# Optimization experiments

Hardware: AMD Instinct MI355X
Metric: run time of the kernel (lower is better)

Reference implementation:

```python
import jax, jax.numpy as jnp
import numpy as np

NUM_EXPERTS = 8
TOP_K = 2
HIDDEN = 2048
INTER = 2816  # 2*INTER = 5632 fused gate+up
NUM_TOKENS = 8192


def setup_inputs() -> dict:
    key = jax.random.key(0)
    k1, k2, k3, k4 = jax.random.split(key, 4)
    hidden_states = jax.random.normal(k1, (NUM_TOKENS, HIDDEN), dtype=jnp.float32)
    gate_w = jax.random.normal(k2, (NUM_EXPERTS, HIDDEN), dtype=jnp.float32) * 0.02
    w13 = jax.random.normal(k3, (NUM_EXPERTS, 2 * INTER, HIDDEN), dtype=jnp.float32) * 0.02
    w2 = jax.random.normal(k4, (NUM_EXPERTS, HIDDEN, INTER), dtype=jnp.float32) * 0.02
    return {"hidden_states": hidden_states, "gate_w": gate_w, "w13": w13, "w2": w2}


def reference(hidden_states, gate_w, w13, w2):
    x = hidden_states  # [T, H]
    # Gate: ReplicatedLinear (no bias) -> router logits [T, E]
    router_logits = jnp.einsum('th,eh->te', x, gate_w)
    probs = jax.nn.softmax(router_logits, axis=-1)
    # top-k routing, renormalize=False: use softmax probs directly
    topk_vals, topk_idx = jax.lax.top_k(probs, TOP_K)  # [T, K]
    # combine weights [T, E]: sum of one-hot(topk_idx) * topk_vals
    cw = jnp.sum(jax.nn.one_hot(topk_idx, NUM_EXPERTS, dtype=x.dtype) * topk_vals[..., None], axis=1)
    # Dense per-expert grouped GEMM, masked combine (E is small and fixed)
    out = jnp.zeros_like(x)
    for e in range(NUM_EXPERTS):
        gu = jnp.einsum('th,ih->ti', x, w13[e])          # [T, 2I]
        g, u = gu[:, :INTER], gu[:, INTER:]
        h = jax.nn.silu(g) * u                            # SiLU-gated
        y = jnp.einsum('ti,hi->th', h, w2[e])             # [T, H]
        out = out + cw[:, e:e + 1] * y
    return out
```

## Files before the change

### kernel.cpp

```cpp
#include <hip/hip_runtime.h>
#include <stdint.h>
#include <stddef.h>

#define NE 8
#define HIDDEN 2048
#define INTER 2816
#define NT 8192
#define NROWS (NT * 2)

typedef __bf16 bf16x8 __attribute__((ext_vector_type(8)));
typedef float f32x4 __attribute__((ext_vector_type(4)));

__device__ __forceinline__ unsigned short f2bf(float f) {
  union { float f; uint32_t u; } v; v.f = f;
  uint32_t r = v.u + 0x7FFFu + ((v.u >> 16) & 1u);
  return (unsigned short)(r >> 16);
}

__device__ __forceinline__ void async16(const void* g, const unsigned short* lds_ptr) {
  __builtin_amdgcn_global_load_lds(
      (const __attribute__((address_space(1))) uint32_t*)g,
      (__attribute__((address_space(3))) uint32_t*)lds_ptr,
      16, 0, 0);
}

__global__ void cvt_kernel(const float4* __restrict__ src, ushort4* __restrict__ dst) {
  size_t i = (size_t)blockIdx.x * blockDim.x + threadIdx.x;
  float4 v = src[i];
  ushort4 o;
  o.x = f2bf(v.x); o.y = f2bf(v.y); o.z = f2bf(v.z); o.w = f2bf(v.w);
  dst[i] = o;
}

__global__ __launch_bounds__(256) void router_kernel(
    const float* __restrict__ x, const float* __restrict__ gw,
    int* __restrict__ top_e, float* __restrict__ top_w, int* __restrict__ counts) {
  int t = blockIdx.x * 4 + (threadIdx.x >> 6);
  int lane = threadIdx.x & 63;
  const float* xr = x + (size_t)t * HIDDEN;
  float acc[NE];
#pragma unroll
  for (int e = 0; e < NE; ++e) acc[e] = 0.f;
  for (int kb = 0; kb < HIDDEN; kb += 64) {
    float xv = xr[kb + lane];
#pragma unroll
    for (int e = 0; e < NE; ++e) acc[e] += xv * gw[e * HIDDEN + kb + lane];
  }
#pragma unroll
  for (int e = 0; e < NE; ++e) {
#pragma unroll
    for (int off = 32; off > 0; off >>= 1) acc[e] += __shfl_xor(acc[e], off, 64);
  }
  if (lane == 0) {
    float mx = acc[0];
#pragma unroll
    for (int e = 1; e < NE; ++e) mx = fmaxf(mx, acc[e]);
    float p[NE];
    float s = 0.f;
#pragma unroll
    for (int e = 0; e < NE; ++e) { p[e] = expf(acc[e] - mx); s += p[e]; }
    int e1 = 0;
#pragma unroll
    for (int e = 1; e < NE; ++e) if (p[e] > p[e1]) e1 = e;
    int e2 = (e1 == 0) ? 1 : 0;
#pragma unroll
    for (int e = 0; e < NE; ++e) if (e != e1 && p[e] > p[e2]) e2 = e;
    float inv = 1.f / s;
    top_e[2 * t] = e1; top_e[2 * t + 1] = e2;
    top_w[2 * t] = p[e1] * inv; top_w[2 * t + 1] = p[e2] * inv;
    atomicAdd(&counts[e1], 1);
    atomicAdd(&counts[e2], 1);
  }
}

__global__ void scan_kernel(const int* __restrict__ counts, int* __restrict__ offs) {
  if (threadIdx.x == 0) {
    int s = 0;
    for (int e = 0; e < NE; ++e) { offs[e] = s; s += counts[e]; }
    offs[NE] = s;
  }
}

__global__ void fill_kernel(const int* __restrict__ top_e, const float* __restrict__ top_w,
                            const int* __restrict__ offs, int* __restrict__ fillc,
                            int* __restrict__ row_tok, float* __restrict__ row_w,
                            int* __restrict__ row_of) {
  int t = blockIdx.x * 256 + threadIdx.x;
#pragma unroll
  for (int j = 0; j < 2; ++j) {
    int e = top_e[2 * t + j];
    int slot = atomicAdd(&fillc[e], 1);
    int row = offs[e] + slot;
    row_tok[row] = t;
    row_w[row] = top_w[2 * t + j];
    row_of[2 * t + j] = row;
  }
}

__global__ __launch_bounds__(512, 2) void gemm1_kernel(
    const unsigned short* __restrict__ xb, const unsigned short* __restrict__ w13b,
    const int* __restrict__ row_tok, const int* __restrict__ offs,
    unsigned short* __restrict__ hbuf) {
  __shared__ __align__(16) unsigned short smem[2][2][16384];
  const int e = blockIdx.z, mt = blockIdx.y, nt = blockIdx.x;
  const int row0 = offs[e];
  const int cnt = offs[e + 1] - row0;
  if (mt * 256 >= cnt) return;
  const int tid = threadIdx.x;

  const int lrow = tid >> 2;
  const int gch = ((tid & 3) ^ ((lrow >> 1) & 3)) * 8;
  size_t aA[2];
#pragma unroll
  for (int i = 0; i < 2; ++i) {
    int grow = mt * 256 + i * 128 + lrow;
    int rr = row0 + (grow < cnt ? grow : cnt - 1);
    aA[i] = (size_t)row_tok[rr] * HIDDEN + gch;
  }
  const size_t aBg = ((size_t)e * 2 * INTER + nt * 128 + lrow) * (size_t)HIDDEN + gch;
  const size_t aBu = ((size_t)e * 2 * INTER + INTER + nt * 128 + lrow) * (size_t)HIDDEN + gch;

  const int wv = tid >> 6, wm = wv >> 1, wn = wv & 1;
  const int l = tid & 63, lm = l & 15, lq = l >> 4;
  const int loff = lm * 32 + ((lq ^ ((lm >> 1) & 3)) * 8);

  f32x4 accg[4][4], accu[4][4];
#pragma unroll
  for (int i = 0; i < 4; ++i)
#pragma unroll
    for (int j = 0; j < 4; ++j) {
      accg[i][j] = (f32x4){0.f, 0.f, 0.f, 0.f};
      accu[i][j] = (f32x4){0.f, 0.f, 0.f, 0.f};
    }

#define ST_A1(NB, KH, KT) do { \
    size_t ko = (size_t)(KT) * 64 + (KH) * 32; \
    async16(xb + aA[0] + ko, &smem[NB][KH][tid * 8]); \
    async16(xb + aA[1] + ko, &smem[NB][KH][4096 + tid * 8]); } while (0)
#define ST_B1(NB, KH, KT) do { \
    size_t ko = (size_t)(KT) * 64 + (KH) * 32; \
    async16(w13b + aBg + ko, &smem[NB][KH][8192 + tid * 8]); \
    async16(w13b + aBu + ko, &smem[NB][KH][12288 + tid * 8]); } while (0)

  ST_A1(0, 0, 0); ST_B1(0, 0, 0); ST_A1(0, 1, 0); ST_B1(0, 1, 0);
  asm volatile("s_waitcnt vmcnt(4)" ::: "memory");
  __builtin_amdgcn_s_barrier();

  const int NTK = HIDDEN / 64;
  for (int t = 0; t < NTK; ++t) {
    const int b = t & 1, nb = b ^ 1;
    const bool pf = (t + 1 < NTK);
#pragma unroll
    for (int kk = 0; kk < 2; ++kk) {
      const unsigned short* sK = &smem[b][kk][0];
      bf16x8 af[4], bfr[4];
#pragma unroll
      for (int i = 0; i < 4; ++i)
        af[i] = *(const bf16x8*)(sK + (wm * 64 + i * 16) * 32 + loff);
#pragma unroll
      for (int j = 0; j < 4; ++j)
        bfr[j] = *(const bf16x8*)(sK + (256 + wn * 64 + j * 16) * 32 + loff);
      if (pf) ST_A1(nb, kk, t + 1);
      __builtin_amdgcn_s_barrier();
      asm volatile("s_waitcnt lgkmcnt(0)" ::: "memory");
      __builtin_amdgcn_sched_barrier(0);
      __builtin_amdgcn_s_setprio(1);
#pragma unroll
      for (int i = 0; i < 4; ++i)
#pragma unroll
        for (int j = 0; j < 4; ++j)
          accg[i][j] = __builtin_amdgcn_mfma_f32_16x16x32_bf16(af[i], bfr[j], accg[i][j], 0, 0, 0);
      __builtin_amdgcn_s_setprio(0);
      __builtin_amdgcn_s_barrier();
#pragma unroll
      for (int j = 0; j < 4; ++j)
        bfr[j] = *(const bf16x8*)(sK + (384 + wn * 64 + j * 16) * 32 + loff);
      if (pf) ST_B1(nb, kk, t + 1);
      if (kk == 0) {
        if (pf) { asm volatile("s_waitcnt vmcnt(4)" ::: "memory"); }
        else    { asm volatile("s_waitcnt vmcnt(0)" ::: "memory"); }
      } else if (pf) {
        asm volatile("s_waitcnt vmcnt(4)" ::: "memory");
      }
      __builtin_amdgcn_s_barrier();
      asm volatile("s_waitcnt lgkmcnt(0)" ::: "memory");
      __builtin_amdgcn_sched_barrier(0);
      __builtin_amdgcn_s_setprio(1);
#pragma unroll
      for (int i = 0; i < 4; ++i)
#pragma unroll
        for (int j = 0; j < 4; ++j)
          accu[i][j] = __builtin_amdgcn_mfma_f32_16x16x32_bf16(af[i], bfr[j], accu[i][j], 0, 0, 0);
      __builtin_amdgcn_s_setprio(0);
      __builtin_amdgcn_s_barrier();
    }
  }
#undef ST_A1
#undef ST_B1

#pragma unroll
  for (int i = 0; i < 4; ++i) {
#pragma unroll
    for (int r = 0; r < 4; ++r) {
      int grow = mt * 256 + wm * 64 + i * 16 + lq * 4 + r;
      if (grow < cnt) {
        size_t hrow = (size_t)(row0 + grow) * INTER + nt * 128 + wn * 64 + lm;
#pragma unroll
        for (int j = 0; j < 4; ++j) {
          float g = accg[i][j][r], u = accu[i][j][r];
          float sg = g / (1.f + expf(-g));
          hbuf[hrow + j * 16] = f2bf(sg * u);
        }
      }
    }
  }
}

__global__ __launch_bounds__(512, 2) void gemm2_kernel(
    const unsigned short* __restrict__ hbuf, const unsigned short* __restrict__ w2b,
    const float* __restrict__ row_w, const int* __restrict__ offs,
    float* __restrict__ ybuf) {
  __shared__ __align__(16) unsigned short smem[2][2][16384];
  const int e = blockIdx.z, mt = blockIdx.y, nt = blockIdx.x;
  const int row0 = offs[e];
  const int cnt = offs[e + 1] - row0;
  if (mt * 256 >= cnt) return;
  const int tid = threadIdx.x;

  const int lrow = tid >> 2;
  const int gch = ((tid & 3) ^ ((lrow >> 1) & 3)) * 8;
  size_t aA[2], aB[2];
#pragma unroll
  for (int i = 0; i < 2; ++i) {
    int grow = mt * 256 + i * 128 + lrow;
    int rr = row0 + (grow < cnt ? grow : cnt - 1);
    aA[i] = (size_t)rr * INTER + gch;
    aB[i] = ((size_t)e * HIDDEN + nt * 256 + i * 128 + lrow) * (size_t)INTER + gch;
  }

  const int wv = tid >> 6, wm = wv >> 1, wn = wv & 1;
  const int l = tid & 63, lm = l & 15, lq = l >> 4;
  const int loff = lm * 32 + ((lq ^ ((lm >> 1) & 3)) * 8);

  f32x4 acc[4][8];
#pragma unroll
  for (int i = 0; i < 4; ++i)
#pragma unroll
    for (int j = 0; j < 8; ++j) acc[i][j] = (f32x4){0.f, 0.f, 0.f, 0.f};

#define ST_A2(NB, KH, KT) do { \
    size_t ko = (size_t)(KT) * 64 + (KH) * 32; \
    async16(hbuf + aA[0] + ko, &smem[NB][KH][tid * 8]); \
    async16(hbuf + aA[1] + ko, &smem[NB][KH][4096 + tid * 8]); } while (0)
#define ST_B2(NB, KH, KT) do { \
    size_t ko = (size_t)(KT) * 64 + (KH) * 32; \
    async16(w2b + aB[0] + ko, &smem[NB][KH][8192 + tid * 8]); \
    async16(w2b + aB[1] + ko, &smem[NB][KH][12288 + tid * 8]); } while (0)

  ST_A2(0, 0, 0); ST_B2(0, 0, 0); ST_A2(0, 1, 0); ST_B2(0, 1, 0);
  asm volatile("s_waitcnt vmcnt(4)" ::: "memory");
  __builtin_amdgcn_s_barrier();

  const int NTK = INTER / 64;
  for (int t = 0; t < NTK; ++t) {
    const int b = t & 1, nb = b ^ 1;
    const bool pf = (t + 1 < NTK);
#pragma unroll
    for (int kk = 0; kk < 2; ++kk) {
      const unsigned short* sK = &smem[b][kk][0];
      bf16x8 af[4], bfr[4];
#pragma unroll
      for (int i = 0; i < 4; ++i)
        af[i] = *(const bf16x8*)(sK + (wm * 64 + i * 16) * 32 + loff);
#pragma unroll
      for (int j = 0; j < 4; ++j)
        bfr[j] = *(const bf16x8*)(sK + (256 + wn * 128 + j * 16) * 32 + loff);
      if (pf) ST_A2(nb, kk, t + 1);
      __builtin_amdgcn_s_barrier();
      asm volatile("s_waitcnt lgkmcnt(0)" ::: "memory");
      __builtin_amdgcn_sched_barrier(0);
      __builtin_amdgcn_s_setprio(1);
#pragma unroll
      for (int i = 0; i < 4; ++i)
#pragma unroll
        for (int j = 0; j < 4; ++j)
          acc[i][j] = __builtin_amdgcn_mfma_f32_16x16x32_bf16(af[i], bfr[j], acc[i][j], 0, 0, 0);
      __builtin_amdgcn_s_setprio(0);
      __builtin_amdgcn_s_barrier();
#pragma unroll
      for (int j = 0; j < 4; ++j)
        bfr[j] = *(const bf16x8*)(sK + (256 + wn * 128 + (j + 4) * 16) * 32 + loff);
      if (pf) ST_B2(nb, kk, t + 1);
      if (kk == 0) {
        if (pf) { asm volatile("s_waitcnt vmcnt(4)" ::: "memory"); }
        else    { asm volatile("s_waitcnt vmcnt(0)" ::: "memory"); }
      } else if (pf) {
        asm volatile("s_waitcnt vmcnt(4)" ::: "memory");
      }
      __builtin_amdgcn_s_barrier();
      asm volatile("s_waitcnt lgkmcnt(0)" ::: "memory");
      __builtin_amdgcn_sched_barrier(0);
      __builtin_amdgcn_s_setprio(1);
#pragma unroll
      for (int i = 0; i < 4; ++i)
#pragma unroll
        for (int j = 0; j < 4; ++j)
          acc[i][j + 4] = __builtin_amdgcn_mfma_f32_16x16x32_bf16(af[i], bfr[j], acc[i][j + 4], 0, 0, 0);
      __builtin_amdgcn_s_setprio(0);
      __builtin_amdgcn_s_barrier();
    }
  }
#undef ST_A2
#undef ST_B2

#pragma unroll
  for (int i = 0; i < 4; ++i) {
#pragma unroll
    for (int r = 0; r < 4; ++r) {
      int grow = mt * 256 + wm * 64 + i * 16 + lq * 4 + r;
      if (grow < cnt) {
        int rr = row0 + grow;
        float w = row_w[rr];
        float* yrow = ybuf + (size_t)rr * HIDDEN + nt * 256 + wn * 128 + lm;
#pragma unroll
        for (int j = 0; j < 8; ++j) yrow[j * 16] = w * acc[i][j][r];
      }
    }
  }
}

__global__ __launch_bounds__(256) void combine_kernel(
    const float* __restrict__ ybuf, const int* __restrict__ row_of,
    float* __restrict__ out) {
  int t = blockIdx.x;
  int r0 = row_of[2 * t], r1 = row_of[2 * t + 1];
  const float4* y0 = (const float4*)(ybuf + (size_t)r0 * HIDDEN);
  const float4* y1 = (const float4*)(ybuf + (size_t)r1 * HIDDEN);
  float4* o = (float4*)(out + (size_t)t * HIDDEN);
#pragma unroll
  for (int it = 0; it < 2; ++it) {
    int c = it * 256 + threadIdx.x;
    float4 a = y0[c], b = y1[c];
    o[c] = make_float4(a.x + b.x, a.y + b.y, a.z + b.z, a.w + b.w);
  }
}

extern "C" void kernel_launch(void* const* d_in, const int* in_sizes, int n_in,
                              void* d_out, int out_size, void* d_ws, size_t ws_size,
                              hipStream_t stream) {
  const float* x = (const float*)d_in[0];
  const float* gw = (const float*)d_in[1];
  const float* w13 = (const float*)d_in[2];
  const float* w2 = (const float*)d_in[3];
  float* out = (float*)d_out;
  char* ws = (char*)d_ws;

  int* counts = (int*)(ws + 0);
  int* fillc = (int*)(ws + 32);
  int* offs = (int*)(ws + 64);
  int* top_e = (int*)(ws + 1024);
  float* top_w = (float*)(ws + 66560);
  int* row_tok = (int*)(ws + 132096);
  float* row_w = (float*)(ws + 197632);
  int* row_of = (int*)(ws + 263168);
  unsigned short* xb = (unsigned short*)(ws + 328704);
  unsigned short* w13b = (unsigned short*)(ws + 33883136);
  float* ybuf = (float*)(ws + 33883136);
  unsigned short* w2b = (unsigned short*)(ws + 218432512);
  unsigned short* hb = (unsigned short*)(ws + 310707200);

  hipMemsetAsync(ws, 0, 1024, stream);

  cvt_kernel<<<16384, 256, 0, stream>>>((const float4*)x, (ushort4*)xb);
  cvt_kernel<<<90112, 256, 0, stream>>>((const float4*)w13, (ushort4*)w13b);
  cvt_kernel<<<45056, 256, 0, stream>>>((const float4*)w2, (ushort4*)w2b);

  router_kernel<<<2048, 256, 0, stream>>>(x, gw, top_e, top_w, counts);
  scan_kernel<<<1, 64, 0, stream>>>(counts, offs);
  fill_kernel<<<32, 256, 0, stream>>>(top_e, top_w, offs, fillc, row_tok, row_w, row_of);

  gemm1_kernel<<<dim3(22, 32, 8), 512, 0, stream>>>(xb, w13b, row_tok, offs, hb);
  gemm2_kernel<<<dim3(8, 32, 8), 512, 0, stream>>>(hb, w2b, row_w, offs, ybuf);
  combine_kernel<<<8192, 256, 0, stream>>>(ybuf, row_of, out);
}
```

Before: 1.644 ms.

## Switch both GEMM mainloops to a 4-stage ring buffer with prefetch three slices ahead

```diff
diff --git a/kernel.cpp b/kernel.cpp
--- a/kernel.cpp
+++ b/kernel.cpp
@@ -101,7 +101,7 @@
     const unsigned short* __restrict__ xb, const unsigned short* __restrict__ w13b,
     const int* __restrict__ row_tok, const int* __restrict__ offs,
     unsigned short* __restrict__ hbuf) {
-  __shared__ __align__(16) unsigned short smem[2][2][16384];
+  __shared__ __align__(16) unsigned short smem[4][16384];
   const int e = blockIdx.z, mt = blockIdx.y, nt = blockIdx.x;
   const int row0 = offs[e];
   const int cnt = offs[e + 1] - row0;
@@ -133,67 +133,60 @@
       accu[i][j] = (f32x4){0.f, 0.f, 0.f, 0.f};
     }
 
-#define ST_A1(NB, KH, KT) do { \
-    size_t ko = (size_t)(KT) * 64 + (KH) * 32; \
-    async16(xb + aA[0] + ko, &smem[NB][KH][tid * 8]); \
-    async16(xb + aA[1] + ko, &smem[NB][KH][4096 + tid * 8]); } while (0)
-#define ST_B1(NB, KH, KT) do { \
-    size_t ko = (size_t)(KT) * 64 + (KH) * 32; \
-    async16(w13b + aBg + ko, &smem[NB][KH][8192 + tid * 8]); \
-    async16(w13b + aBu + ko, &smem[NB][KH][12288 + tid * 8]); } while (0)
-
-  ST_A1(0, 0, 0); ST_B1(0, 0, 0); ST_A1(0, 1, 0); ST_B1(0, 1, 0);
-  asm volatile("s_waitcnt vmcnt(4)" ::: "memory");
+#define ST_A1(P) do { \
+    size_t ko = (size_t)(P) * 32; unsigned short* sD = &smem[(P) & 3][0]; \
+    async16(xb + aA[0] + ko, sD + tid * 8); \
+    async16(xb + aA[1] + ko, sD + 4096 + tid * 8); } while (0)
+#define ST_B1(P) do { \
+    size_t ko = (size_t)(P) * 32; unsigned short* sD = &smem[(P) & 3][0]; \
+    async16(w13b + aBg + ko, sD + 8192 + tid * 8); \
+    async16(w13b + aBu + ko, sD + 12288 + tid * 8); } while (0)
+
+  const int NP = HIDDEN / 32;
+  ST_A1(0); ST_B1(0); ST_A1(1); ST_B1(1); ST_A1(2); ST_B1(2);
+  asm volatile("s_waitcnt vmcnt(8)" ::: "memory");
   __builtin_amdgcn_s_barrier();
 
-  const int NTK = HIDDEN / 64;
-  for (int t = 0; t < NTK; ++t) {
-    const int b = t & 1, nb = b ^ 1;
-    const bool pf = (t + 1 < NTK);
-#pragma unroll
-    for (int kk = 0; kk < 2; ++kk) {
-      const unsigned short* sK = &smem[b][kk][0];
-      bf16x8 af[4], bfr[4];
-#pragma unroll
-      for (int i = 0; i < 4; ++i)
-        af[i] = *(const bf16x8*)(sK + (wm * 64 + i * 16) * 32 + loff);
+  for (int p = 0; p < NP; ++p) {
+    const unsigned short* sK = &smem[p & 3][0];
+    const bool pf = (p + 3 < NP);
+    bf16x8 af[4], bfr[4];
+#pragma unroll
+    for (int i = 0; i < 4; ++i)
+      af[i] = *(const bf16x8*)(sK + (wm * 64 + i * 16) * 32 + loff);
+#pragma unroll
+    for (int j = 0; j < 4; ++j)
+      bfr[j] = *(const bf16x8*)(sK + (256 + wn * 64 + j * 16) * 32 + loff);
+    if (pf) ST_A1(p + 3);
+    __builtin_amdgcn_s_barrier();
+    asm volatile("s_waitcnt lgkmcnt(0)" ::: "memory");
+    __builtin_amdgcn_sched_barrier(0);
+    __builtin_amdgcn_s_setprio(1);
+#pragma unroll
+    for (int i = 0; i < 4; ++i)
 #pragma unroll
       for (int j = 0; j < 4; ++j)
-        bfr[j] = *(const bf16x8*)(sK + (256 + wn * 64 + j * 16) * 32 + loff);
-      if (pf) ST_A1(nb, kk, t + 1);
-      __builtin_amdgcn_s_barrier();
-      asm volatile("s_waitcnt lgkmcnt(0)" ::: "memory");
-      __builtin_amdgcn_sched_barrier(0);
-      __builtin_amdgcn_s_setprio(1);
-#pragma unroll
-      for (int i = 0; i < 4; ++i)
-#pragma unroll
-        for (int j = 0; j < 4; ++j)
-          accg[i][j] = __builtin_amdgcn_mfma_f32_16x16x32_bf16(af[i], bfr[j], accg[i][j], 0, 0, 0);
-      __builtin_amdgcn_s_setprio(0);
-      __builtin_amdgcn_s_barrier();
+        accg[i][j] = __builtin_amdgcn_mfma_f32_16x16x32_bf16(af[i], bfr[j], accg[i][j], 0, 0, 0);
+    __builtin_amdgcn_s_setprio(0);
+    __builtin_amdgcn_s_barrier();
+#pragma unroll
+    for (int j = 0; j < 4; ++j)
+      bfr[j] = *(const bf16x8*)(sK + (384 + wn * 64 + j * 16) * 32 + loff);
+    if (pf) ST_B1(p + 3);
+    if (pf)                  { asm volatile("s_waitcnt vmcnt(8)" ::: "memory"); }
+    else if (p + 2 < NP)     { asm volatile("s_waitcnt vmcnt(4)" ::: "memory"); }
+    else                     { asm volatile("s_waitcnt vmcnt(0)" ::: "memory"); }
+    __builtin_amdgcn_s_barrier();
+    asm volatile("s_waitcnt lgkmcnt(0)" ::: "memory");
+    __builtin_amdgcn_sched_barrier(0);
+    __builtin_amdgcn_s_setprio(1);
+#pragma unroll
+    for (int i = 0; i < 4; ++i)
 #pragma unroll
       for (int j = 0; j < 4; ++j)
-        bfr[j] = *(const bf16x8*)(sK + (384 + wn * 64 + j * 16) * 32 + loff);
-      if (pf) ST_B1(nb, kk, t + 1);
-      if (kk == 0) {
-        if (pf) { asm volatile("s_waitcnt vmcnt(4)" ::: "memory"); }
-        else    { asm volatile("s_waitcnt vmcnt(0)" ::: "memory"); }
-      } else if (pf) {
-        asm volatile("s_waitcnt vmcnt(4)" ::: "memory");
-      }
-      __builtin_amdgcn_s_barrier();
-      asm volatile("s_waitcnt lgkmcnt(0)" ::: "memory");
-      __builtin_amdgcn_sched_barrier(0);
-      __builtin_amdgcn_s_setprio(1);
-#pragma unroll
-      for (int i = 0; i < 4; ++i)
-#pragma unroll
-        for (int j = 0; j < 4; ++j)
-          accu[i][j] = __builtin_amdgcn_mfma_f32_16x16x32_bf16(af[i], bfr[j], accu[i][j], 0, 0, 0);
-      __builtin_amdgcn_s_setprio(0);
-      __builtin_amdgcn_s_barrier();
-    }
+        accu[i][j] = __builtin_amdgcn_mfma_f32_16x16x32_bf16(af[i], bfr[j], accu[i][j], 0, 0, 0);
+    __builtin_amdgcn_s_setprio(0);
+    __builtin_amdgcn_s_barrier();
   }
 #undef ST_A1
 #undef ST_B1
@@ -220,7 +213,7 @@
     const unsigned short* __restrict__ hbuf, const unsigned short* __restrict__ w2b,
     const float* __restrict__ row_w, const int* __restrict__ offs,
     float* __restrict__ ybuf) {
-  __shared__ __align__(16) unsigned short smem[2][2][16384];
+  __shared__ __align__(16) unsigned short smem[4][16384];
   const int e = blockIdx.z, mt = blockIdx.y, nt = blockIdx.x;
   const int row0 = offs[e];
   const int cnt = offs[e + 1] - row0;
@@ -248,67 +241,60 @@
 #pragma unroll
     for (int j = 0; j < 8; ++j) acc[i][j] = (f32x4){0.f, 0.f, 0.f, 0.f};
 
-#define ST_A2(NB, KH, KT) do { \
-    size_t ko = (size_t)(KT) * 64 + (KH) * 32; \
-    async16(hbuf + aA[0] + ko, &smem[NB][KH][tid * 8]); \
-    async16(hbuf + aA[1] + ko, &smem[NB][KH][4096 + tid * 8]); } while (0)
-#define ST_B2(NB, KH, KT) do { \
-    size_t ko = (size_t)(KT) * 64 + (KH) * 32; \
-    async16(w2b + aB[0] + ko, &smem[NB][KH][8192 + tid * 8]); \
-    async16(w2b + aB[1] + ko, &smem[NB][KH][12288 + tid * 8]); } while (0)
-
-  ST_A2(0, 0, 0); ST_B2(0, 0, 0); ST_A2(0, 1, 0); ST_B2(0, 1, 0);
-  asm volatile("s_waitcnt vmcnt(4)" ::: "memory");
+#define ST_A2(P) do { \
+    size_t ko = (size_t)(P) * 32; unsigned short* sD = &smem[(P) & 3][0]; \
+    async16(hbuf + aA[0] + ko, sD + tid * 8); \
+    async16(hbuf + aA[1] + ko, sD + 4096 + tid * 8); } while (0)
+#define ST_B2(P) do { \
+    size_t ko = (size_t)(P) * 32; unsigned short* sD = &smem[(P) & 3][0]; \
+    async16(w2b + aB[0] + ko, sD + 8192 + tid * 8); \
+    async16(w2b + aB[1] + ko, sD + 12288 + tid * 8); } while (0)
+
+  const int NP = INTER / 32;
+  ST_A2(0); ST_B2(0); ST_A2(1); ST_B2(1); ST_A2(2); ST_B2(2);
+  asm volatile("s_waitcnt vmcnt(8)" ::: "memory");
   __builtin_amdgcn_s_barrier();
 
-  const int NTK = INTER / 64;
-  for (int t = 0; t < NTK; ++t) {
-    const int b = t & 1, nb = b ^ 1;
-    const bool pf = (t + 1 < NTK);
-#pragma unroll
-    for (int kk = 0; kk < 2; ++kk) {
-      const unsigned short* sK = &smem[b][kk][0];
-      bf16x8 af[4], bfr[4];
-#pragma unroll
-      for (int i = 0; i < 4; ++i)
-        af[i] = *(const bf16x8*)(sK + (wm * 64 + i * 16) * 32 + loff);
+  for (int p = 0; p < NP; ++p) {
+    const unsigned short* sK = &smem[p & 3][0];
+    const bool pf = (p + 3 < NP);
+    bf16x8 af[4], bfr[4];
+#pragma unroll
+    for (int i = 0; i < 4; ++i)
+      af[i] = *(const bf16x8*)(sK + (wm * 64 + i * 16) * 32 + loff);
+#pragma unroll
+    for (int j = 0; j < 4; ++j)
+      bfr[j] = *(const bf16x8*)(sK + (256 + wn * 128 + j * 16) * 32 + loff);
+    if (pf) ST_A2(p + 3);
+    __builtin_amdgcn_s_barrier();
+    asm volatile("s_waitcnt lgkmcnt(0)" ::: "memory");
+    __builtin_amdgcn_sched_barrier(0);
+    __builtin_amdgcn_s_setprio(1);
+#pragma unroll
+    for (int i = 0; i < 4; ++i)
 #pragma unroll
       for (int j = 0; j < 4; ++j)
-        bfr[j] = *(const bf16x8*)(sK + (256 + wn * 128 + j * 16) * 32 + loff);
-      if (pf) ST_A2(nb, kk, t + 1);
-      __builtin_amdgcn_s_barrier();
-      asm volatile("s_waitcnt lgkmcnt(0)" ::: "memory");
-      __builtin_amdgcn_sched_barrier(0);
-      __builtin_amdgcn_s_setprio(1);
-#pragma unroll
-      for (int i = 0; i < 4; ++i)
-#pragma unroll
-        for (int j = 0; j < 4; ++j)
-          acc[i][j] = __builtin_amdgcn_mfma_f32_16x16x32_bf16(af[i], bfr[j], acc[i][j], 0, 0, 0);
-      __builtin_amdgcn_s_setprio(0);
-      __builtin_amdgcn_s_barrier();
+        acc[i][j] = __builtin_amdgcn_mfma_f32_16x16x32_bf16(af[i], bfr[j], acc[i][j], 0, 0, 0);
+    __builtin_amdgcn_s_setprio(0);
+    __builtin_amdgcn_s_barrier();
+#pragma unroll
+    for (int j = 0; j < 4; ++j)
+      bfr[j] = *(const bf16x8*)(sK + (256 + wn * 128 + (j + 4) * 16) * 32 + loff);
+    if (pf) ST_B2(p + 3);
+    if (pf)                  { asm volatile("s_waitcnt vmcnt(8)" ::: "memory"); }
+    else if (p + 2 < NP)     { asm volatile("s_waitcnt vmcnt(4)" ::: "memory"); }
+    else                     { asm volatile("s_waitcnt vmcnt(0)" ::: "memory"); }
+    __builtin_amdgcn_s_barrier();
+    asm volatile("s_waitcnt lgkmcnt(0)" ::: "memory");
+    __builtin_amdgcn_sched_barrier(0);
+    __builtin_amdgcn_s_setprio(1);
+#pragma unroll
+    for (int i = 0; i < 4; ++i)
 #pragma unroll
       for (int j = 0; j < 4; ++j)
-        bfr[j] = *(const bf16x8*)(sK + (256 + wn * 128 + (j + 4) * 16) * 32 + loff);
-      if (pf) ST_B2(nb, kk, t + 1);
-      if (kk == 0) {
-        if (pf) { asm volatile("s_waitcnt vmcnt(4)" ::: "memory"); }
-        else    { asm volatile("s_waitcnt vmcnt(0)" ::: "memory"); }
-      } else if (pf) {
-        asm volatile("s_waitcnt vmcnt(4)" ::: "memory");
-      }
-      __builtin_amdgcn_s_barrier();
-      asm volatile("s_waitcnt lgkmcnt(0)" ::: "memory");
-      __builtin_amdgcn_sched_barrier(0);
-      __builtin_amdgcn_s_setprio(1);
-#pragma unroll
-      for (int i = 0; i < 4; ++i)
-#pragma unroll
-        for (int j = 0; j < 4; ++j)
-          acc[i][j + 4] = __builtin_amdgcn_mfma_f32_16x16x32_bf16(af[i], bfr[j], acc[i][j + 4], 0, 0, 0);
-      __builtin_amdgcn_s_setprio(0);
-      __builtin_amdgcn_s_barrier();
-    }
+        acc[i][j + 4] = __builtin_amdgcn_mfma_f32_16x16x32_bf16(af[i], bfr[j], acc[i][j + 4], 0, 0, 0);
+    __builtin_amdgcn_s_setprio(0);
+    __builtin_amdgcn_s_barrier();
   }
 #undef ST_A2
 #undef ST_B2
```

Measured after the change: 1.675 ms. About the same (+1.9%).
